# Performance work log

Hardware: AMD Instinct MI355X
Metric: run time of the kernel (lower is better)

## Reference

```python
import jax, jax.numpy as jnp
import numpy as np

B, S, H, NH, HD = 1, 2048, 768, 12, 64   # batch, seq, hidden, heads, head_dim
W = 256                                   # one-sided window (attention_window=512)
NC = S // W                               # query chunks of width W
L, FF, V, G = 12, 3072, 50265, 1          # layers, ffn, vocab, num global tokens (CLS)
HID, EMB = 768, 256                       # head dense size, output embedding size
SCALE = 1.0 / np.sqrt(HD).astype(np.float32)
EPS = 1e-5

def _ln(x, s, b):
    mu = x.mean(-1, keepdims=True)
    xm = x - mu
    v = (xm * xm).mean(-1, keepdims=True)
    return xm * jax.lax.rsqrt(v + EPS) * s + b

def _forward(input_ids, attention_mask, global_attention_mask,
             word_emb, pos_emb, emb_ln_s, emb_ln_b,
             Wq, bq, Wk, bk, Wv, bv, Wqg, bqg, Wkg, bkg, Wvg, bvg, Wo, bo,
             ln1_s, ln1_b, Wf1, bf1, Wf2, bf2, ln2_s, ln2_b,
             dense_w, dense_b, out_w, out_b):
    h = word_emb[input_ids] + pos_emb[None]            # [B,S,H]
    h = _ln(h, emb_ln_s, emb_ln_b)

    key_ok = attention_mask.astype(bool)               # [B,S]
    is_glb = global_attention_mask.astype(bool)        # [B,S]

    # chunked sliding-window machinery: queries in NC chunks of W, each sees 3W keys
    j = jnp.arange(3 * W); qi = jnp.arange(W); c = jnp.arange(NC)
    rel = j[None, :] - qi[:, None]
    band_ok = (rel >= 0) & (rel <= 2 * W)              # |key-query| <= W  -> [W,3W]
    kpos = c[:, None, None] * W + j[None, None, :] - W # abs key position [NC,1,3W]
    in_range = (kpos >= 0) & (kpos < S)
    kposc = jnp.clip(kpos, 0, S - 1)
    # HF removes global tokens from the windowed band (they get dedicated columns)
    kmask = key_ok[:, kposc] & ~is_glb[:, kposc]       # [B,NC,1,3W]
    band_mask = band_ok[None, None] & in_range[None] & kmask          # [B,NC,W,3W]
    gcol_mask = jnp.broadcast_to(key_ok[:, None, None, :G], (B, NC, W, G))
    full_mask = jnp.concatenate([gcol_mask, band_mask], -1)[:, None]  # [B,1,NC,W,G+3W]
    kidx = c[:, None] * W + j[None, :]                 # gather into padded keys [NC,3W]

    def step(h, p):
        q = ((h @ p['Wq'] + p['bq']).reshape(B, NC, W, NH, HD)) * SCALE
        k = (h @ p['Wk'] + p['bk']).reshape(B, S, NH, HD)
        v = (h @ p['Wv'] + p['bv']).reshape(B, S, NH, HD)
        k_ch = jnp.pad(k, ((0, 0), (W, W), (0, 0), (0, 0)))[:, kidx]  # [B,NC,3W,NH,HD]
        v_ch = jnp.pad(v, ((0, 0), (W, W), (0, 0), (0, 0)))[:, kidx]
        s_band = jnp.einsum('bcqnd,bcknd->bncqk', q, k_ch)            # [B,NH,NC,W,3W]
        s_glob = jnp.einsum('bcqnd,bgnd->bncqg', q, k[:, :G])         # [B,NH,NC,W,G]
        scores = jnp.concatenate([s_glob, s_band], -1)
        probs = jax.nn.softmax(jnp.where(full_mask, scores, -1e9), -1)
        pg, pb = probs[..., :G], probs[..., G:]
        out = (jnp.einsum('bncqk,bcknd->bcqnd', pb, v_ch)
               + jnp.einsum('bncqg,bgnd->bcqnd', pg, v[:, :G]))
        out = out.reshape(B, S, NH, HD)
        # global tokens: full attention with dedicated global projections (HF semantics)
        hg = h[:, :G]
        qg = ((hg @ p['Wqg'] + p['bqg']).reshape(B, G, NH, HD)) * SCALE
        kg = (h @ p['Wkg'] + p['bkg']).reshape(B, S, NH, HD)
        vg = (h @ p['Wvg'] + p['bvg']).reshape(B, S, NH, HD)
        sg = jnp.einsum('bgnd,bsnd->bngs', qg, kg)
        ag = jax.nn.softmax(jnp.where(key_ok[:, None, None, :], sg, -1e9), -1)
        og = jnp.einsum('bngs,bsnd->bgnd', ag, vg)
        out = out.at[:, :G].set(og)
        attn = out.reshape(B, S, H) @ p['Wo'] + p['bo']
        h2 = _ln(h + attn, p['ln1_s'], p['ln1_b'])
        ff = jax.nn.gelu(h2 @ p['Wf1'] + p['bf1'], approximate=False) @ p['Wf2'] + p['bf2']
        return _ln(h2 + ff, p['ln2_s'], p['ln2_b']), None

    params = dict(Wq=Wq, bq=bq, Wk=Wk, bk=bk, Wv=Wv, bv=bv, Wqg=Wqg, bqg=bqg,
                  Wkg=Wkg, bkg=bkg, Wvg=Wvg, bvg=bvg, Wo=Wo, bo=bo,
                  ln1_s=ln1_s, ln1_b=ln1_b, Wf1=Wf1, bf1=bf1, Wf2=Wf2, bf2=bf2,
                  ln2_s=ln2_s, ln2_b=ln2_b)
    h, _ = jax.lax.scan(step, h, params)
    pooled = h[:, 0]                                   # CLS token
    y = jnp.tanh(pooled @ dense_w + dense_b)           # dropout = identity (eval)
    return y @ out_w + out_b                           # [B,EMB]

def setup_inputs() -> dict:
    key = jax.random.key(0)
    it = iter(jax.random.split(key, 16))
    def nrm(shape, sd=0.02):
        return jax.random.normal(next(it), shape, jnp.float32) * sd
    return dict(
        input_ids=jax.random.randint(next(it), (B, S), 0, V),
        attention_mask=jnp.ones((B, S), jnp.int32),
        global_attention_mask=jnp.zeros((B, S), jnp.int32).at[:, 0].set(1),
        word_emb=nrm((V, H)), pos_emb=nrm((S, H)),
        emb_ln_s=jnp.ones((H,)), emb_ln_b=jnp.zeros((H,)),
        Wq=nrm((L, H, H)), bq=jnp.zeros((L, H)),
        Wk=nrm((L, H, H)), bk=jnp.zeros((L, H)),
        Wv=nrm((L, H, H)), bv=jnp.zeros((L, H)),
        Wqg=nrm((L, H, H)), bqg=jnp.zeros((L, H)),
        Wkg=nrm((L, H, H)), bkg=jnp.zeros((L, H)),
        Wvg=nrm((L, H, H)), bvg=jnp.zeros((L, H)),
        Wo=nrm((L, H, H)), bo=jnp.zeros((L, H)),
        ln1_s=jnp.ones((L, H)), ln1_b=jnp.zeros((L, H)),
        Wf1=nrm((L, H, FF)), bf1=jnp.zeros((L, FF)),
        Wf2=nrm((L, FF, H)), bf2=jnp.zeros((L, H)),
        ln2_s=jnp.ones((L, H)), ln2_b=jnp.zeros((L, H)),
        dense_w=nrm((H, HID)), dense_b=jnp.zeros((HID,)),
        out_w=nrm((HID, EMB)), out_b=jnp.zeros((EMB,)),
    )

def reference(input_ids, attention_mask, global_attention_mask,
              word_emb, pos_emb, emb_ln_s, emb_ln_b,
              Wq, bq, Wk, bk, Wv, bv, Wqg, bqg, Wkg, bkg, Wvg, bvg, Wo, bo,
              ln1_s, ln1_b, Wf1, bf1, Wf2, bf2, ln2_s, ln2_b,
              dense_w, dense_b, out_w, out_b):
    return _forward(input_ids, attention_mask, global_attention_mask,
                    word_emb, pos_emb, emb_ln_s, emb_ln_b,
                    Wq, bq, Wk, bk, Wv, bv, Wqg, bqg, Wkg, bkg, Wvg, bvg, Wo, bo,
                    ln1_s, ln1_b, Wf1, bf1, Wf2, bf2, ln2_s, ln2_b,
                    dense_w, dense_b, out_w, out_b)
```

## Files before the change

### kernel.cpp

```cpp
#include <hip/hip_runtime.h>
#include <hip/hip_bf16.h>

typedef __hip_bfloat16 bf16;
using bf16x8 = __attribute__((ext_vector_type(8))) short;
using f32x4  = __attribute__((ext_vector_type(4))) float;

#define kNEG 1.0e9f

__device__ __forceinline__ float b2f(bf16 x){ return __bfloat162float(x); }
__device__ __forceinline__ bf16  f2b(float x){ return __float2bfloat16(x); }
__device__ __forceinline__ float us2f(unsigned short u){ return __uint_as_float(((unsigned)u)<<16); }

__device__ __forceinline__ float erf_fast(float z){
  float az = fabsf(z);
  float t = __frcp_rn(fmaf(0.3275911f, az, 1.0f));
  float p = t*fmaf(t, fmaf(t, fmaf(t, fmaf(t, 1.061405429f, -1.453152027f),
                                    1.421413741f), -0.284496736f), 0.254829592f);
  float e = 1.0f - p*__expf(-az*az);
  return copysignf(e, z);
}

#define GLDS16(gp, lp) __builtin_amdgcn_global_load_lds( \
    (const __attribute__((address_space(1))) void*)(gp), \
    (__attribute__((address_space(3))) void*)(lp), 16, 0, 0)

__device__ __forceinline__ void unpack8(uint4 u, float* f){
  f[0]=__uint_as_float(u.x<<16); f[1]=__uint_as_float(u.x&0xffff0000u);
  f[2]=__uint_as_float(u.y<<16); f[3]=__uint_as_float(u.y&0xffff0000u);
  f[4]=__uint_as_float(u.z<<16); f[5]=__uint_as_float(u.z&0xffff0000u);
  f[6]=__uint_as_float(u.w<<16); f[7]=__uint_as_float(u.w&0xffff0000u);
}

__global__ __launch_bounds__(192)
void embed_ln(const int* __restrict__ ids, const float* __restrict__ wemb,
              const float* __restrict__ pemb, const float* __restrict__ lns,
              const float* __restrict__ lnb, float* __restrict__ hout,
              bf16* __restrict__ hbout)
{
  const int row = blockIdx.x;
  const int tid = threadIdx.x;
  const int wave = tid >> 6, lane = tid & 63;
  const int id = ids[row];
  const int i0 = tid*4;
  float4 a = *(const float4*)&wemb[(size_t)id*768 + i0];
  float4 b = *(const float4*)&pemb[(size_t)row*768 + i0];
  float4 x = make_float4(a.x+b.x, a.y+b.y, a.z+b.z, a.w+b.w);
  float s1 = x.x+x.y+x.z+x.w;
  float s2 = x.x*x.x+x.y*x.y+x.z*x.z+x.w*x.w;
  #pragma unroll
  for (int m=32;m>=1;m>>=1){ s1 += __shfl_xor(s1,m); s2 += __shfl_xor(s2,m); }
  __shared__ float red[6];
  if (lane==0){ red[wave]=s1; red[3+wave]=s2; }
  __syncthreads();
  s1 = red[0]+red[1]+red[2];
  s2 = red[3]+red[4]+red[5];
  float mu = s1*(1.0f/768.0f);
  float var = s2*(1.0f/768.0f) - mu*mu;
  float rs = rsqrtf(var + 1e-5f);
  float4 sc = *(const float4*)&lns[i0];
  float4 bi = *(const float4*)&lnb[i0];
  float4 y = make_float4((x.x-mu)*rs*sc.x + bi.x, (x.y-mu)*rs*sc.y + bi.y,
                         (x.z-mu)*rs*sc.z + bi.z, (x.w-mu)*rs*sc.w + bi.w);
  *(float4*)&hout[(size_t)row*768 + i0] = y;
  union { ushort4 u; bf16 h[4]; } pk;
  pk.h[0]=f2b(y.x); pk.h[1]=f2b(y.y); pk.h[2]=f2b(y.z); pk.h[3]=f2b(y.w);
  *(ushort4*)&hbout[(size_t)row*768 + i0] = pk.u;
}

template<int NP>
__global__ __launch_bounds__(192)
void add_ln(const float* __restrict__ res, const bf16* __restrict__ pf,
            const float* __restrict__ lns, const float* __restrict__ lnb,
            float* __restrict__ hout, bf16* __restrict__ hbout)
{
  const size_t MN = (size_t)2048*768;
  const int row = blockIdx.x;
  const int tid = threadIdx.x;
  const int wave = tid >> 6, lane = tid & 63;
  const int i0 = tid*4;
  const size_t base = (size_t)row*768 + i0;
  float4 x = *(const float4*)&res[base];
  #pragma unroll
  for (int p=0;p<NP;p++){
    ushort4 u = *(const ushort4*)&pf[p*MN + base];
    x.x += us2f(u.x); x.y += us2f(u.y); x.z += us2f(u.z); x.w += us2f(u.w);
  }
  float s1 = x.x+x.y+x.z+x.w;
  float s2 = x.x*x.x+x.y*x.y+x.z*x.z+x.w*x.w;
  #pragma unroll
  for (int m=32;m>=1;m>>=1){ s1 += __shfl_xor(s1,m); s2 += __shfl_xor(s2,m); }
  __shared__ float red[6];
  if (lane==0){ red[wave]=s1; red[3+wave]=s2; }
  __syncthreads();
  s1 = red[0]+red[1]+red[2];
  s2 = red[3]+red[4]+red[5];
  float mu = s1*(1.0f/768.0f);
  float var = s2*(1.0f/768.0f) - mu*mu;
  float rs = rsqrtf(var + 1e-5f);
  float4 sc = *(const float4*)&lns[i0];
  float4 bi = *(const float4*)&lnb[i0];
  float4 y = make_float4((x.x-mu)*rs*sc.x + bi.x, (x.y-mu)*rs*sc.y + bi.y,
                         (x.z-mu)*rs*sc.z + bi.z, (x.w-mu)*rs*sc.w + bi.w);
  *(float4*)&hout[base] = y;
  union { ushort4 u; bf16 h[4]; } pk;
  pk.h[0]=f2b(y.x); pk.h[1]=f2b(y.y); pk.h[2]=f2b(y.z); pk.h[3]=f2b(y.w);
  *(ushort4*)&hbout[base] = pk.u;
}

__global__ __launch_bounds__(256)
void prep_all(const float* __restrict__ Wq, const float* __restrict__ Wk,
              const float* __restrict__ Wv, const float* __restrict__ Wkg,
              const float* __restrict__ Wvg, const float* __restrict__ Wo,
              const float* __restrict__ Wf1, const float* __restrict__ Wf2,
              const float* __restrict__ bq, const float* __restrict__ bk,
              const float* __restrict__ bv, const float* __restrict__ bkg,
              const float* __restrict__ bvg,
              bf16* __restrict__ WcatT, bf16* __restrict__ WoT,
              bf16* __restrict__ Wf1T, bf16* __restrict__ Wf2T,
              float* __restrict__ bcat)
{
  const int b = blockIdx.x;
  const int l = blockIdx.y;
  const int tid = threadIdx.x;
  const size_t oHH = (size_t)l*768*768;
  const size_t oHF = (size_t)l*768*3072;
  const size_t oH  = (size_t)l*768;
  if (b >= 504) {
    int i = (b-504)*256 + tid;
    int which = i / 768, j = i - which*768;
    float v;
    if      (which==0) v = bq[oH+j] * 0.125f;
    else if (which==1) v = bk[oH+j];
    else if (which==2) v = bv[oH+j];
    else if (which==3) v = bkg[oH+j];
    else               v = bvg[oH+j];
    bcat[(size_t)l*3840 + i] = v;
    return;
  }
  const float* src; bf16* dst; int N, KT64, p0, tk, k0, n0; float scale = 1.0f;
  if (b < 180) {
    int wsel = b/36, tile = b - wsel*36;
    int tkk = tile/3, tn = tile - tkk*3;
    if      (wsel==0){ src=Wq+oHH;  scale=0.125f; }
    else if (wsel==1){ src=Wk+oHH; }
    else if (wsel==2){ src=Wv+oHH; }
    else if (wsel==3){ src=Wkg+oHH; }
    else             { src=Wvg+oHH; }
    dst = WcatT + (size_t)l*5*768*768;
    N=768; KT64=12; k0=tkk*64; n0=tn*256; p0 = wsel*6 + tn*2; tk = tkk;
  } else if (b < 216) {
    int tile = b-180, tkk = tile/3, tn = tile - tkk*3;
    src = Wo+oHH; dst = WoT + (size_t)l*768*768;
    N=768; KT64=12; k0=tkk*64; n0=tn*256; p0 = tn*2; tk = tkk;
  } else if (b < 360) {
    int tile = b-216, tkk = tile/12, tn = tile - tkk*12;
    src = Wf1+oHF; dst = Wf1T + (size_t)l*768*3072;
    N=3072; KT64=12; k0=tkk*64; n0=tn*256; p0 = tn*2; tk = tkk;
  } else {
    int tile = b-360, tkk = tile/3, tn = tile - tkk*3;
    src = Wf2+oHF; dst = Wf2T + (size_t)l*768*3072;
    N=768; KT64=48; k0=tkk*64; n0=tn*256; p0 = tn*2; tk = tkk;
  }

  __shared__ bf16 t[64][264];
  const int wave = tid>>6, lane = tid&63;
  float4 v[16];
  #pragma unroll
  for (int i=0;i<16;i++){
    int r = i*4 + wave;
    v[i] = *(const float4*)&src[(size_t)(k0+r)*N + n0 + lane*4];
  }
  #pragma unroll
  for (int i=0;i<16;i++){
    int r = i*4 + wave;
    union { ushort4 u; bf16 h[4]; } pk;
    pk.h[0]=f2b(v[i].x*scale); pk.h[1]=f2b(v[i].y*scale);
    pk.h[2]=f2b(v[i].z*scale); pk.h[3]=f2b(v[i].w*scale);
    *(ushort4*)&t[r][lane*4] = pk.u;
  }
  __syncthreads();
  const int rr = tid>>1, half = tid&1;
  const int r7 = rr & 7;
  #pragma unroll
  for (int c=0;c<4;c++){
    const int pp = c>>1, tt = c&1;
    union { uint4 u[2]; bf16 h[16]; } pk;
    #pragma unroll
    for (int j=0;j<16;j++)
      pk.h[j] = t[tt*32 + half*16 + j][pp*128 + rr];
    bf16* base = dst + ((size_t)(p0+pp)*KT64 + tk)*8192 + rr*64;
    const int g0 = tt*4 + half*2;
    *(uint4*)(base + (((g0  ) ^ r7)<<3)) = pk.u[0];
    *(uint4*)(base + (((g0+1) ^ r7)<<3)) = pk.u[1];
  }
}

template<int OUTF, int OUTB, int GELU, int KSPLIT, int VT>
__global__ __launch_bounds__(256)
void gemm_bt(const bf16* __restrict__ A, const bf16* __restrict__ Bt,
             const float* __restrict__ bias,
             bf16* __restrict__ pfb, bf16* __restrict__ outb,
             bf16* __restrict__ vt,
             int M, int N, int K)
{
  __shared__ bf16 As[2][128*64];
  __shared__ bf16 Bs[2][128*64];
  const int tid  = threadIdx.x;
  const int lane = tid & 63;
  const int wave = tid >> 6;
  const int wm = wave >> 1, wn = wave & 1;
  const int gx = gridDim.x, nwg = gx*gridDim.y;
  const int w  = blockIdx.y*gx + blockIdx.x;
  const int cpx = nwg >> 3;
  const int sw = (w & 7)*cpx + (w >> 3);
  const int bm = sw % gx, bn = sw / gx;
  const int bz = (KSPLIT>1) ? blockIdx.z : 0;
  const int fr = lane & 15;
  const int fk = lane >> 4;
  const int x7 = fr & 7;
  const int Ks = K / KSPLIT;
  const int nt = Ks >> 6;
  const int kbeg = bz * Ks;
  const int KT64 = K >> 6;

  const bf16* pa[4];
  int ldsA[4];
  #pragma unroll
  for (int i=0;i<4;i++){
    int s = i*256 + tid;
    int row = s >> 3, k8l = s & 7;
    pa[i] = A + (size_t)(bm*128 + row)*K + kbeg + ((k8l ^ (row&7))<<3);
    ldsA[i] = s*8;
  }
  const bf16* pB = Bt + ((size_t)bn*KT64 + (kbeg>>6))*8192;

  f32x4 acc[4][4];
  const f32x4 zero = {0.f,0.f,0.f,0.f};
  #pragma unroll
  for (int i=0;i<4;i++)
    #pragma unroll
    for (int j=0;j<4;j++) acc[i][j] = zero;

  #pragma unroll
  for (int i=0;i<4;i++) GLDS16(pa[i], &As[0][ldsA[i]]);
  #pragma unroll
  for (int i=0;i<4;i++){ int o=(i*256+tid)*8; GLDS16(pB+o, &Bs[0][o]); }
  if (nt > 1) {
    #pragma unroll
    for (int i=0;i<4;i++) GLDS16(pa[i]+64, &As[1][ldsA[i]]);
    #pragma unroll
    for (int i=0;i<4;i++){ int o=(i*256+tid)*8; GLDS16(pB+8192+o, &Bs[1][o]); }
  }

  for (int t = 0; t < nt; ++t) {
    const int cur = t & 1;
    if (t < nt-1) asm volatile("s_waitcnt vmcnt(8)" ::: "memory");
    else          asm volatile("s_waitcnt vmcnt(0)" ::: "memory");
    __builtin_amdgcn_s_barrier();
    __builtin_amdgcn_sched_barrier(0);

    bf16x8 af[2][4], bfr[2][4];
    #pragma unroll
    for (int kk=0;kk<2;kk++){
      #pragma unroll
      for (int m=0;m<4;m++)
        af[kk][m] = *reinterpret_cast<const bf16x8*>(
            &As[cur][(wm*64 + m*16 + fr)*64 + ((((kk<<2)+fk) ^ x7)<<3)]);
      #pragma unroll
      for (int n=0;n<4;n++)
        bfr[kk][n] = *reinterpret_cast<const bf16x8*>(
            &Bs[cur][(wn*64 + n*16 + fr)*64 + ((((kk<<2)+fk) ^ x7)<<3)]);
    }
    __builtin_amdgcn_s_setprio(1);
    #pragma unroll
    for (int kk=0;kk<2;kk++)
      #pragma unroll
      for (int m=0;m<4;m++)
        #pragma unroll
        for (int n=0;n<4;n++)
          acc[m][n] = __builtin_amdgcn_mfma_f32_16x16x32_bf16(af[kk][m], bfr[kk][n], acc[m][n], 0,0,0);
    __builtin_amdgcn_s_setprio(0);

    __builtin_amdgcn_s_barrier();
    __builtin_amdgcn_sched_barrier(0);
    if (t+2 < nt) {
      #pragma unroll
      for (int i=0;i<4;i++) GLDS16(pa[i] + (size_t)(t+2)*64, &As[cur][ldsA[i]]);
      #pragma unroll
      for (int i=0;i<4;i++){ int o=(i*256+tid)*8;
        GLDS16(pB + (size_t)(t+2)*8192 + o, &Bs[cur][o]); }
    }
  }

  const int row0 = bm*128 + wm*64 + (lane>>4)*4;
  const int col0 = bn*128 + wn*64 + fr;
  bf16* pfz = OUTF ? (pfb + (size_t)bz*M*N) : nullptr;
  #pragma unroll
  for (int n=0;n<4;n++){
    const int col = col0 + n*16;
    const float bv = (bz==0) ? bias[col] : 0.f;
    #pragma unroll
    for (int m=0;m<4;m++){
      const int r0 = row0 + m*16;
      union { ushort4 u; bf16 h[4]; } pk;
      #pragma unroll
      for (int r=0;r<4;r++){
        float x = acc[m][n][r] + bv;
        if (GELU) x = 0.5f*x*(1.0f + erf_fast(x*0.70710678118f));
        size_t idx = (size_t)(r0+r)*N + col;
        pk.h[r] = f2b(x);
        if (OUTF) pfz[idx] = pk.h[r];
        if (OUTB) outb[idx] = pk.h[r];
      }
      if (VT) {
        if (col >= 1536 && col < 2304)
          *(ushort4*)&vt[(size_t)(col-1536)*2048 + r0] = pk.u;
      }
    }
  }
}

__global__ __launch_bounds__(256)
void band_attn(const bf16* __restrict__ qkv, const bf16* __restrict__ Vt,
               const float* __restrict__ h0, const float* __restrict__ Wqg,
               const float* __restrict__ bqg,
               const int* __restrict__ amask, const int* __restrict__ gmask,
               bf16* __restrict__ attn)
{
  const int c = blockIdx.x, n = blockIdx.y, rg = blockIdx.z;
  const int tid = threadIdx.x, wave = tid>>6, lane = tid&63;

  if (rg == 4) {
    if (c != 0) return;
    __shared__ float sg[2048];
    __shared__ float qh[64];
    __shared__ float redg[8];
    __shared__ float partg[4][64];
    {
      const int d = tid & 63;
      const int w = tid >> 6;
      const float* wp = Wqg + (size_t)(w*192)*768 + n*64 + d;
      float a = 0.f;
      #pragma unroll 8
      for (int k=0;k<192;k++) a += h0[w*192+k] * wp[(size_t)k*768];
      partg[w][d] = a;
    }
    __syncthreads();
    if (tid < 64)
      qh[tid] = (partg[0][tid]+partg[1][tid]+partg[2][tid]+partg[3][tid] + bqg[n*64+tid]) * 0.125f;
    __syncthreads();

    float smax = -3.0e38f;
    for (int p=0;p<8;p++){
      int s = p*256 + tid;
      const uint4* kr = (const uint4*)(qkv + (size_t)s*3840 + 2304 + n*64);
      float acc = 0.f;
      #pragma unroll
      for (int d8=0; d8<8; d8++){
        float f[8]; unpack8(kr[d8], f);
        #pragma unroll
        for (int e=0;e<8;e++) acc += f[e]*qh[d8*8+e];
      }
      if (amask[s] == 0) acc = -kNEG;
      sg[s] = acc;
      smax = fmaxf(smax, acc);
    }
    #pragma unroll
    for (int mk=32; mk>=1; mk>>=1) smax = fmaxf(smax, __shfl_xor(smax, mk));
    if (lane==0) redg[wave] = smax;
    __syncthreads();
    smax = fmaxf(fmaxf(redg[0],redg[1]),fmaxf(redg[2],redg[3]));
    float ssum = 0.f;
    for (int p=0;p<8;p++){
      int s = p*256 + tid;
      float e = __expf(sg[s]-smax);
      sg[s] = e;
      ssum += e;
    }
    #pragma unroll
    for (int mk=32; mk>=1; mk>>=1) ssum += __shfl_xor(ssum, mk);
    if (lane==0) redg[4+wave] = ssum;
    __syncthreads();
    float total = redg[4]+redg[5]+redg[6]+redg[7];
    __syncthreads();

    float o0=0.f,o1=0.f,o2=0.f,o3=0.f;
    const int base = wave*512;
    for (int s = base; s < base+512; s+=4){
      o0 += sg[s]   * b2f(qkv[(size_t)s*3840     + 3072 + n*64 + lane]);
      o1 += sg[s+1] * b2f(qkv[(size_t)(s+1)*3840 + 3072 + n*64 + lane]);
      o2 += sg[s+2] * b2f(qkv[(size_t)(s+2)*3840 + 3072 + n*64 + lane]);
      o3 += sg[s+3] * b2f(qkv[(size_t)(s+3)*3840 + 3072 + n*64 + lane]);
    }
    partg[wave][lane] = (o0+o1)+(o2+o3);
    __syncthreads();
    if (tid < 64) {
      float oo = (partg[0][tid]+partg[1][tid]+partg[2][tid]+partg[3][tid]) / total;
      attn[n*64+tid] = f2b(oo);
    }
    return;
  }

  const int fr = lane & 15, fk = lane >> 4;
  const int jj = tid >> 2, seg = tid & 3;

  __shared__ __attribute__((aligned(16))) bf16 q_s[64][72];
  __shared__ __attribute__((aligned(16))) bf16 k_s[2][64][72];
  __shared__ __attribute__((aligned(16))) bf16 vt_s[2][64][72];
  __shared__ __attribute__((aligned(16))) bf16 p_s[4][16][72];
  __shared__ int  okk_s[768];
  __shared__ float kv0[2][64];

  {
    const uint4* src = (const uint4*)(qkv + (size_t)(c*256 + rg*64 + jj)*3840 + n*64 + seg*16);
    *(uint4*)&q_s[jj][seg*16]   = src[0];
    *(uint4*)&q_s[jj][seg*16+8] = src[1];
  }
  #pragma unroll
  for (int p=0;p<3;p++){
    int j = tid + p*256;
    int kpos = c*256 + j - 256;
    int ok = 0;
    if (kpos >= 0 && kpos < 2048) ok = (amask[kpos] != 0) && (gmask[kpos] == 0);
    okk_s[j] = ok;
  }
  if (tid < 64)       kv0[0][tid]    = b2f(qkv[768  + n*64 + tid]);
  else if (tid < 128) kv0[1][tid-64] = b2f(qkv[1536 + n*64 + (tid-64)]);

  auto loadK = [&](int kt, uint4& a, uint4& b){
    int kpos = c*256 + kt*64 + jj - 256;
    int kq = kpos < 0 ? 0 : (kpos > 2047 ? 2047 : kpos);
    const uint4* ks = (const uint4*)(qkv + (size_t)kq*3840 + 768 + n*64 + seg*16);
    a = ks[0]; b = ks[1];
  };
  auto loadV = [&](int kt, uint4& a, uint4& b){
    int base = c*256 + kt*64 - 256;
    int sb = (base < 0 || base > 2048-64) ? 0 : base;
    const uint4* vs = (const uint4*)(Vt + (size_t)(n*64 + jj)*2048 + sb + seg*8);
    a = vs[0]; b = vs[4];
  };

  const int kt_lo = (c==0) ? ((rg > 4) ? rg : 4) : rg;
  int kt_hi = rg+8 < 11 ? rg+8 : 11;
  const int clip = (2303 - c*256) >> 6;
  if (kt_hi > clip) kt_hi = clip;

  uint4 ka,kb,va,vb;
  loadK(kt_lo,ka,kb); loadV(kt_lo,va,vb);
  *(uint4*)&k_s[0][jj][seg*16]    = ka;
  *(uint4*)&k_s[0][jj][seg*16+8]  = kb;
  *(uint4*)&vt_s[0][jj][seg*8]    = va;
  *(uint4*)&vt_s[0][jj][seg*8+32] = vb;

  float lsum[4];
  f32x4 out[4];
  const f32x4 zero = {0.f,0.f,0.f,0.f};
  #pragma unroll
  for (int r=0;r<4;r++) lsum[r] = 0.f;
  #pragma unroll
  for (int dt=0;dt<4;dt++) out[dt] = zero;

  int cur = 0;
  for (int kt = kt_lo; kt <= kt_hi; kt++) {
    const bool pf = (kt < kt_hi);
    if (pf){ loadK(kt+1,ka,kb); loadV(kt+1,va,vb); }
    __syncthreads();

    f32x4 s[4];
    #pragma unroll
    for (int ct=0;ct<4;ct++) s[ct] = zero;
    __builtin_amdgcn_s_setprio(1);
    #pragma unroll
    for (int ks=0;ks<2;ks++){
      bf16x8 aq = *reinterpret_cast<const bf16x8*>(&q_s[wave*16 + fr][ks*32 + fk*8]);
      #pragma unroll
      for (int ct=0;ct<4;ct++){
        bf16x8 bk = *reinterpret_cast<const bf16x8*>(&k_s[cur][ct*16 + fr][ks*32 + fk*8]);
        s[ct] = __builtin_amdgcn_mfma_f32_16x16x32_bf16(aq, bk, s[ct], 0,0,0);
      }
    }
    __builtin_amdgcn_s_setprio(0);
    const int qbase = rg*64 + wave*16 + fk*4;
    #pragma unroll
    for (int ct=0;ct<4;ct++){
      int j = kt*64 + ct*16 + fr;
      int okj = okk_s[j];
      #pragma unroll
      for (int r=0;r<4;r++){
        unsigned rel = (unsigned)(j - (qbase + r));
        float sv = (okj && rel <= 512u) ? s[ct][r] : -kNEG;
        float p = __expf(sv);
        lsum[r] += p;
        p_s[wave][fk*4 + r][ct*16 + fr] = f2b(p);
      }
    }
    __builtin_amdgcn_s_setprio(1);
    #pragma unroll
    for (int ks=0;ks<2;ks++){
      bf16x8 ap = *reinterpret_cast<const bf16x8*>(&p_s[wave][fr][ks*32 + fk*8]);
      #pragma unroll
      for (int dt=0;dt<4;dt++){
        bf16x8 bv = *reinterpret_cast<const bf16x8*>(&vt_s[cur][dt*16 + fr][ks*32 + fk*8]);
        out[dt] = __builtin_amdgcn_mfma_f32_16x16x32_bf16(ap, bv, out[dt], 0,0,0);
      }
    }
    __builtin_amdgcn_s_setprio(0);

    if (pf){
      *(uint4*)&k_s[cur^1][jj][seg*16]    = ka;
      *(uint4*)&k_s[cur^1][jj][seg*16+8]  = kb;
      *(uint4*)&vt_s[cur^1][jj][seg*8]    = va;
      *(uint4*)&vt_s[cur^1][jj][seg*8+32] = vb;
      cur ^= 1;
    }
  }

  const bool okg = (amask[0] != 0);
  #pragma unroll
  for (int r=0;r<4;r++){
    const int row16 = fk*4 + r;
    float ts = lsum[r];
    #pragma unroll
    for (int mk=8; mk>=1; mk>>=1) ts += __shfl_xor(ts, mk);
    float sp = 0.f;
    #pragma unroll
    for (int e=0;e<4;e++){
      int d = fr*4 + e;
      sp += b2f(q_s[wave*16 + row16][d]) * kv0[0][d];
    }
    #pragma unroll
    for (int mk=8; mk>=1; mk>>=1) sp += __shfl_xor(sp, mk);
    float pg = okg ? __expf(sp) : 0.f;
    float lf = ts + pg;
    const int srow = c*256 + rg*64 + wave*16 + row16;
    if (srow != 0) {
      #pragma unroll
      for (int dt=0;dt<4;dt++){
        int d = dt*16 + fr;
        float o = (out[dt][r] + pg*kv0[1][d]) / lf;
        attn[(size_t)srow*768 + n*64 + d] = f2b(o);
      }
    }
  }
}

__global__ __launch_bounds__(256)
void head_p1(const float* __restrict__ h0, const float* __restrict__ dw,
             float* __restrict__ pd)
{
  const int col = blockIdx.x*256 + threadIdx.x;
  const int z = blockIdx.y;
  const int k0 = z*96;
  float acc = 0.f;
  #pragma unroll 8
  for (int k=0;k<96;k++) acc += h0[k0+k]*dw[(size_t)(k0+k)*768 + col];
  pd[z*768 + col] = acc;
}

__global__ __launch_bounds__(256)
void head_p2(const float* __restrict__ pd, const float* __restrict__ db,
             const float* __restrict__ ow, float* __restrict__ po)
{
  __shared__ float yl[96];
  const int tid = threadIdx.x;
  const int z = blockIdx.x;
  const int k0 = z*96;
  if (tid < 96) {
    float a = 0.f;
    #pragma unroll
    for (int zz=0;zz<8;zz++) a += pd[zz*768 + k0 + tid];
    yl[tid] = tanhf(a + db[k0 + tid]);
  }
  __syncthreads();
  const int col = tid;
  float acc = 0.f;
  #pragma unroll 8
  for (int k=0;k<96;k++) acc += yl[k]*ow[(size_t)(k0+k)*256 + col];
  po[z*256 + col] = acc;
}

__global__ __launch_bounds__(256)
void head_fin(const float* __restrict__ po, const float* __restrict__ ob,
              float* __restrict__ out)
{
  const int col = threadIdx.x;
  float a = 0.f;
  #pragma unroll
  for (int z=0;z<8;z++) a += po[z*256 + col];
  out[col] = a + ob[col];
}

extern "C" void kernel_launch(void* const* d_in, const int* in_sizes, int n_in,
                              void* d_out, int out_size, void* d_ws, size_t ws_size,
                              hipStream_t stream)
{
  const int*   ids   = (const int*)d_in[0];
  const int*   amask = (const int*)d_in[1];
  const int*   gmask = (const int*)d_in[2];
  const float* wemb  = (const float*)d_in[3];
  const float* pemb  = (const float*)d_in[4];
  const float* elns  = (const float*)d_in[5];
  const float* elnb  = (const float*)d_in[6];
  const float* Wq    = (const float*)d_in[7];
  const float* bq    = (const float*)d_in[8];
  const float* Wk    = (const float*)d_in[9];
  const float* bk    = (const float*)d_in[10];
  const float* Wv    = (const float*)d_in[11];
  const float* bv    = (const float*)d_in[12];
  const float* Wqg   = (const float*)d_in[13];
  const float* bqg   = (const float*)d_in[14];
  const float* Wkg   = (const float*)d_in[15];
  const float* bkg   = (const float*)d_in[16];
  const float* Wvg   = (const float*)d_in[17];
  const float* bvg   = (const float*)d_in[18];
  const float* Wo    = (const float*)d_in[19];
  const float* bo    = (const float*)d_in[20];
  const float* ln1s  = (const float*)d_in[21];
  const float* ln1b  = (const float*)d_in[22];
  const float* Wf1   = (const float*)d_in[23];
  const float* bf1   = (const float*)d_in[24];
  const float* Wf2   = (const float*)d_in[25];
  const float* bf2   = (const float*)d_in[26];
  const float* ln2s  = (const float*)d_in[27];
  const float* ln2b  = (const float*)d_in[28];
  const float* dw    = (const float*)d_in[29];
  const float* db    = (const float*)d_in[30];
  const float* ow    = (const float*)d_in[31];
  const float* ob    = (const float*)d_in[32];

  char* ws = (char*)d_ws;
  size_t off = 0;
  auto alloc = [&](size_t bytes)->char*{
    char* p = ws + off; off += (bytes + 255) & ~(size_t)255; return p;
  };
  float* h     = (float*)alloc((size_t)2048*768*4);
  bf16*  hb    = (bf16*) alloc((size_t)2048*768*2);
  float* h2    = (float*)alloc((size_t)2048*768*4);
  bf16*  h2b   = (bf16*) alloc((size_t)2048*768*2);
  bf16*  qkv   = (bf16*) alloc((size_t)2048*3840*2);
  bf16*  att   = (bf16*) alloc((size_t)2048*768*2);
  bf16*  f1    = (bf16*) alloc((size_t)2048*3072*2);
  bf16*  Vtb   = (bf16*) alloc((size_t)768*2048*2);
  bf16*  pfb   = (bf16*) alloc((size_t)4*2048*768*2);
  bf16*  WcatT = (bf16*) alloc((size_t)12*5*768*768*2);
  bf16*  WoT   = (bf16*) alloc((size_t)12*768*768*2);
  bf16*  Wf1T  = (bf16*) alloc((size_t)12*768*3072*2);
  bf16*  Wf2T  = (bf16*) alloc((size_t)12*768*3072*2);
  float* bcat  = (float*)alloc((size_t)12*3840*4);
  float* pd    = (float*)alloc((size_t)8*768*4);
  float* po    = (float*)alloc((size_t)8*256*4);

  prep_all<<<dim3(519,12),256,0,stream>>>(Wq, Wk, Wv, Wkg, Wvg, Wo, Wf1, Wf2,
                                          bq, bk, bv, bkg, bvg,
                                          WcatT, WoT, Wf1T, Wf2T, bcat);
  embed_ln<<<2048,192,0,stream>>>(ids, wemb, pemb, elns, elnb, h, hb);

  for (int l=0; l<12; l++) {
    const size_t oHH = (size_t)l*768*768;
    const size_t oH  = (size_t)l*768;
    const size_t oF  = (size_t)l*3072;
    const bf16* WcatT_l = WcatT + (size_t)l*5*768*768;
    const bf16* WoT_l   = WoT   + (size_t)l*768*768;
    const bf16* Wf1T_l  = Wf1T  + (size_t)l*768*3072;
    const bf16* Wf2T_l  = Wf2T  + (size_t)l*768*3072;
    const float* bcat_l = bcat  + (size_t)l*3840;

    gemm_bt<0,1,0,1,1><<<dim3(16,30),256,0,stream>>>(hb, WcatT_l, bcat_l, nullptr, qkv,
                                                     Vtb, 2048, 3840, 768);
    band_attn<<<dim3(8,12,5),256,0,stream>>>(qkv, Vtb, h, Wqg+oHH, bqg+oH,
                                             amask, gmask, att);
    gemm_bt<1,0,0,3,0><<<dim3(16,6,3),256,0,stream>>>(att, WoT_l, bo+oH, pfb, nullptr,
                                                      nullptr, 2048, 768, 768);
    add_ln<3><<<2048,192,0,stream>>>(h, pfb, ln1s+oH, ln1b+oH, h2, h2b);
    gemm_bt<0,1,1,1,0><<<dim3(16,24),256,0,stream>>>(h2b, Wf1T_l, bf1+oF, nullptr, f1,
                                                     nullptr, 2048, 3072, 768);
    gemm_bt<1,0,0,3,0><<<dim3(16,6,3),256,0,stream>>>(f1, Wf2T_l, bf2+oH, pfb, nullptr,
                                                      nullptr, 2048, 768, 3072);
    add_ln<3><<<2048,192,0,stream>>>(h2, pfb, ln2s+oH, ln2b+oH, h, hb);
  }

  head_p1<<<dim3(3,8),256,0,stream>>>(h, dw, pd);
  head_p2<<<8,256,0,stream>>>(pd, db, ow, po);
  head_fin<<<1,256,0,stream>>>(po, ob, (float*)d_out);
}
```

Baseline: 2.114 ms.

## Fold global K/V projections into the CLS global-attention path

Drops the global key and value projections from the fused QKV GEMM, shrinking it from 3840 to 2304 output columns. The single global query row now gets its scores as h·(Wkg·q) plus a bias constant, and its output as Wvg applied to the softmax-weighted sum of h, all computed inside band_attn. This removes a large share of the per-layer projection GEMM and the matching weight preparation. In exchange, 12 single blocks (one per head) must each stream the full fp32 hidden state twice, which may lengthen band_attn's tail. Accumulation order and precision for the global row also change.

```diff
diff --git a/kernel.cpp b/kernel.cpp
--- a/kernel.cpp
+++ b/kernel.cpp
@@ -23,13 +23,6 @@
 #define GLDS16(gp, lp) __builtin_amdgcn_global_load_lds( \
     (const __attribute__((address_space(1))) void*)(gp), \
     (__attribute__((address_space(3))) void*)(lp), 16, 0, 0)
-
-__device__ __forceinline__ void unpack8(uint4 u, float* f){
-  f[0]=__uint_as_float(u.x<<16); f[1]=__uint_as_float(u.x&0xffff0000u);
-  f[2]=__uint_as_float(u.y<<16); f[3]=__uint_as_float(u.y&0xffff0000u);
-  f[4]=__uint_as_float(u.z<<16); f[5]=__uint_as_float(u.z&0xffff0000u);
-  f[6]=__uint_as_float(u.w<<16); f[7]=__uint_as_float(u.w&0xffff0000u);
-}
 
 __global__ __launch_bounds__(192)
 void embed_ln(const int* __restrict__ ids, const float* __restrict__ wemb,
@@ -109,12 +102,10 @@
 
 __global__ __launch_bounds__(256)
 void prep_all(const float* __restrict__ Wq, const float* __restrict__ Wk,
-              const float* __restrict__ Wv, const float* __restrict__ Wkg,
-              const float* __restrict__ Wvg, const float* __restrict__ Wo,
+              const float* __restrict__ Wv, const float* __restrict__ Wo,
               const float* __restrict__ Wf1, const float* __restrict__ Wf2,
               const float* __restrict__ bq, const float* __restrict__ bk,
-              const float* __restrict__ bv, const float* __restrict__ bkg,
-              const float* __restrict__ bvg,
+              const float* __restrict__ bv,
               bf16* __restrict__ WcatT, bf16* __restrict__ WoT,
               bf16* __restrict__ Wf1T, bf16* __restrict__ Wf2T,
               float* __restrict__ bcat)
@@ -125,39 +116,35 @@
   const size_t oHH = (size_t)l*768*768;
   const size_t oHF = (size_t)l*768*3072;
   const size_t oH  = (size_t)l*768;
-  if (b >= 504) {
-    int i = (b-504)*256 + tid;
+  if (b >= 432) {
+    int i = (b-432)*256 + tid;
     int which = i / 768, j = i - which*768;
     float v;
     if      (which==0) v = bq[oH+j] * 0.125f;
     else if (which==1) v = bk[oH+j];
-    else if (which==2) v = bv[oH+j];
-    else if (which==3) v = bkg[oH+j];
-    else               v = bvg[oH+j];
-    bcat[(size_t)l*3840 + i] = v;
+    else               v = bv[oH+j];
+    bcat[(size_t)l*2304 + i] = v;
     return;
   }
   const float* src; bf16* dst; int N, KT64, p0, tk, k0, n0; float scale = 1.0f;
-  if (b < 180) {
+  if (b < 108) {
     int wsel = b/36, tile = b - wsel*36;
     int tkk = tile/3, tn = tile - tkk*3;
     if      (wsel==0){ src=Wq+oHH;  scale=0.125f; }
     else if (wsel==1){ src=Wk+oHH; }
-    else if (wsel==2){ src=Wv+oHH; }
-    else if (wsel==3){ src=Wkg+oHH; }
-    else             { src=Wvg+oHH; }
-    dst = WcatT + (size_t)l*5*768*768;
+    else             { src=Wv+oHH; }
+    dst = WcatT + (size_t)l*3*768*768;
     N=768; KT64=12; k0=tkk*64; n0=tn*256; p0 = wsel*6 + tn*2; tk = tkk;
-  } else if (b < 216) {
-    int tile = b-180, tkk = tile/3, tn = tile - tkk*3;
+  } else if (b < 144) {
+    int tile = b-108, tkk = tile/3, tn = tile - tkk*3;
     src = Wo+oHH; dst = WoT + (size_t)l*768*768;
     N=768; KT64=12; k0=tkk*64; n0=tn*256; p0 = tn*2; tk = tkk;
-  } else if (b < 360) {
-    int tile = b-216, tkk = tile/12, tn = tile - tkk*12;
+  } else if (b < 288) {
+    int tile = b-144, tkk = tile/12, tn = tile - tkk*12;
     src = Wf1+oHF; dst = Wf1T + (size_t)l*768*3072;
     N=3072; KT64=12; k0=tkk*64; n0=tn*256; p0 = tn*2; tk = tkk;
   } else {
-    int tile = b-360, tkk = tile/3, tn = tile - tkk*3;
+    int tile = b-288, tkk = tile/3, tn = tile - tkk*3;
     src = Wf2+oHF; dst = Wf2T + (size_t)l*768*3072;
     N=768; KT64=48; k0=tkk*64; n0=tn*256; p0 = tn*2; tk = tkk;
   }
@@ -322,8 +309,10 @@
 
 __global__ __launch_bounds__(256)
 void band_attn(const bf16* __restrict__ qkv, const bf16* __restrict__ Vt,
-               const float* __restrict__ h0, const float* __restrict__ Wqg,
-               const float* __restrict__ bqg,
+               const float* __restrict__ h0,
+               const float* __restrict__ Wqg, const float* __restrict__ bqg,
+               const float* __restrict__ Wkg, const float* __restrict__ bkg,
+               const float* __restrict__ Wvg, const float* __restrict__ bvg,
                const int* __restrict__ amask, const int* __restrict__ gmask,
                bf16* __restrict__ attn)
 {
@@ -334,6 +323,7 @@
     if (c != 0) return;
     __shared__ float sg[2048];
     __shared__ float qh[64];
+    __shared__ float wz[768];
     __shared__ float redg[8];
     __shared__ float partg[4][64];
     {
@@ -349,17 +339,29 @@
     if (tid < 64)
       qh[tid] = (partg[0][tid]+partg[1][tid]+partg[2][tid]+partg[3][tid] + bqg[n*64+tid]) * 0.125f;
     __syncthreads();
-
+    for (int k = tid; k < 768; k += 256) {
+      const float4* wr = (const float4*)&Wkg[(size_t)k*768 + n*64];
+      float a = 0.f;
+      #pragma unroll
+      for (int d4=0; d4<16; d4++){
+        float4 w4 = wr[d4];
+        a += w4.x*qh[d4*4+0] + w4.y*qh[d4*4+1] + w4.z*qh[d4*4+2] + w4.w*qh[d4*4+3];
+      }
+      wz[k] = a;
+    }
+    float cst = 0.f;
+    #pragma unroll 8
+    for (int d=0; d<64; d++) cst += bkg[n*64+d]*qh[d];
+    __syncthreads();
     float smax = -3.0e38f;
     for (int p=0;p<8;p++){
       int s = p*256 + tid;
-      const uint4* kr = (const uint4*)(qkv + (size_t)s*3840 + 2304 + n*64);
-      float acc = 0.f;
-      #pragma unroll
-      for (int d8=0; d8<8; d8++){
-        float f[8]; unpack8(kr[d8], f);
-        #pragma unroll
-        for (int e=0;e<8;e++) acc += f[e]*qh[d8*8+e];
+      const float4* hr = (const float4*)&h0[(size_t)s*768];
+      float acc = cst;
+      #pragma unroll 4
+      for (int k4=0;k4<192;k4++){
+        float4 h4 = hr[k4];
+        acc += h4.x*wz[k4*4+0] + h4.y*wz[k4*4+1] + h4.z*wz[k4*4+2] + h4.w*wz[k4*4+3];
       }
       if (amask[s] == 0) acc = -kNEG;
       sg[s] = acc;
@@ -383,19 +385,30 @@
     __syncthreads();
     float total = redg[4]+redg[5]+redg[6]+redg[7];
     __syncthreads();
-
-    float o0=0.f,o1=0.f,o2=0.f,o3=0.f;
-    const int base = wave*512;
-    for (int s = base; s < base+512; s+=4){
-      o0 += sg[s]   * b2f(qkv[(size_t)s*3840     + 3072 + n*64 + lane]);
-      o1 += sg[s+1] * b2f(qkv[(size_t)(s+1)*3840 + 3072 + n*64 + lane]);
-      o2 += sg[s+2] * b2f(qkv[(size_t)(s+2)*3840 + 3072 + n*64 + lane]);
-      o3 += sg[s+3] * b2f(qkv[(size_t)(s+3)*3840 + 3072 + n*64 + lane]);
-    }
-    partg[wave][lane] = (o0+o1)+(o2+o3);
+    float z0=0.f,z1=0.f,z2=0.f,y0=0.f,y1=0.f,y2=0.f;
+    const int kk0 = tid*3;
+    for (int s=0;s<2048;s+=2){
+      float a0 = sg[s], a1 = sg[s+1];
+      const float* r0 = &h0[(size_t)s*768 + kk0];
+      const float* r1 = r0 + 768;
+      z0 = fmaf(a0, r0[0], z0); z1 = fmaf(a0, r0[1], z1); z2 = fmaf(a0, r0[2], z2);
+      y0 = fmaf(a1, r1[0], y0); y1 = fmaf(a1, r1[1], y1); y2 = fmaf(a1, r1[2], y2);
+    }
+    wz[kk0+0] = z0+y0; wz[kk0+1] = z1+y1; wz[kk0+2] = z2+y2;
+    __syncthreads();
+    {
+      const int d = tid & 63;
+      const int w = tid >> 6;
+      const float* wv = Wvg + (size_t)(w*192)*768 + n*64 + d;
+      float a = 0.f;
+      #pragma unroll 8
+      for (int k=0;k<192;k++) a = fmaf(wz[w*192+k], wv[(size_t)k*768], a);
+      partg[w][d] = a;
+    }
     __syncthreads();
     if (tid < 64) {
-      float oo = (partg[0][tid]+partg[1][tid]+partg[2][tid]+partg[3][tid]) / total;
+      float oo = (partg[0][tid]+partg[1][tid]+partg[2][tid]+partg[3][tid]) / total
+               + bvg[n*64+tid];
       attn[n*64+tid] = f2b(oo);
     }
     return;
@@ -412,7 +425,7 @@
   __shared__ float kv0[2][64];
 
   {
-    const uint4* src = (const uint4*)(qkv + (size_t)(c*256 + rg*64 + jj)*3840 + n*64 + seg*16);
+    const uint4* src = (const uint4*)(qkv + (size_t)(c*256 + rg*64 + jj)*2304 + n*64 + seg*16);
     *(uint4*)&q_s[jj][seg*16]   = src[0];
     *(uint4*)&q_s[jj][seg*16+8] = src[1];
   }
@@ -430,7 +443,7 @@
   auto loadK = [&](int kt, uint4& a, uint4& b){
     int kpos = c*256 + kt*64 + jj - 256;
     int kq = kpos < 0 ? 0 : (kpos > 2047 ? 2047 : kpos);
-    const uint4* ks = (const uint4*)(qkv + (size_t)kq*3840 + 768 + n*64 + seg*16);
+    const uint4* ks = (const uint4*)(qkv + (size_t)kq*2304 + 768 + n*64 + seg*16);
     a = ks[0]; b = ks[1];
   };
   auto loadV = [&](int kt, uint4& a, uint4& b){
@@ -637,21 +650,21 @@
   bf16*  hb    = (bf16*) alloc((size_t)2048*768*2);
   float* h2    = (float*)alloc((size_t)2048*768*4);
   bf16*  h2b   = (bf16*) alloc((size_t)2048*768*2);
-  bf16*  qkv   = (bf16*) alloc((size_t)2048*3840*2);
+  bf16*  qkv   = (bf16*) alloc((size_t)2048*2304*2);
   bf16*  att   = (bf16*) alloc((size_t)2048*768*2);
   bf16*  f1    = (bf16*) alloc((size_t)2048*3072*2);
   bf16*  Vtb   = (bf16*) alloc((size_t)768*2048*2);
   bf16*  pfb   = (bf16*) alloc((size_t)4*2048*768*2);
-  bf16*  WcatT = (bf16*) alloc((size_t)12*5*768*768*2);
+  bf16*  WcatT = (bf16*) alloc((size_t)12*3*768*768*2);
   bf16*  WoT   = (bf16*) alloc((size_t)12*768*768*2);
   bf16*  Wf1T  = (bf16*) alloc((size_t)12*768*3072*2);
   bf16*  Wf2T  = (bf16*) alloc((size_t)12*768*3072*2);
-  float* bcat  = (float*)alloc((size_t)12*3840*4);
+  float* bcat  = (float*)alloc((size_t)12*2304*4);
   float* pd    = (float*)alloc((size_t)8*768*4);
   float* po    = (float*)alloc((size_t)8*256*4);
 
-  prep_all<<<dim3(519,12),256,0,stream>>>(Wq, Wk, Wv, Wkg, Wvg, Wo, Wf1, Wf2,
-                                          bq, bk, bv, bkg, bvg,
+  prep_all<<<dim3(441,12),256,0,stream>>>(Wq, Wk, Wv, Wo, Wf1, Wf2,
+                                          bq, bk, bv,
                                           WcatT, WoT, Wf1T, Wf2T, bcat);
   embed_ln<<<2048,192,0,stream>>>(ids, wemb, pemb, elns, elnb, h, hb);
 
@@ -659,15 +672,17 @@
     const size_t oHH = (size_t)l*768*768;
     const size_t oH  = (size_t)l*768;
     const size_t oF  = (size_t)l*3072;
-    const bf16* WcatT_l = WcatT + (size_t)l*5*768*768;
+    const bf16* WcatT_l = WcatT + (size_t)l*3*768*768;
     const bf16* WoT_l   = WoT   + (size_t)l*768*768;
     const bf16* Wf1T_l  = Wf1T  + (size_t)l*768*3072;
     const bf16* Wf2T_l  = Wf2T  + (size_t)l*768*3072;
-    const float* bcat_l = bcat  + (size_t)l*3840;
-
-    gemm_bt<0,1,0,1,1><<<dim3(16,30),256,0,stream>>>(hb, WcatT_l, bcat_l, nullptr, qkv,
-                                                     Vtb, 2048, 3840, 768);
-    band_attn<<<dim3(8,12,5),256,0,stream>>>(qkv, Vtb, h, Wqg+oHH, bqg+oH,
+    const float* bcat_l = bcat  + (size_t)l*2304;
+
+    gemm_bt<0,1,0,1,1><<<dim3(16,18),256,0,stream>>>(hb, WcatT_l, bcat_l, nullptr, qkv,
+                                                     Vtb, 2048, 2304, 768);
+    band_attn<<<dim3(8,12,5),256,0,stream>>>(qkv, Vtb, h,
+                                             Wqg+oHH, bqg+oH, Wkg+oHH, bkg+oH,
+                                             Wvg+oHH, bvg+oH,
                                              amask, gmask, att);
     gemm_bt<1,0,0,3,0><<<dim3(16,6,3),256,0,stream>>>(att, WoT_l, bo+oH, pfb, nullptr,
                                                       nullptr, 2048, 768, 768);
```

Result: slower. 4.933 ms (+133.3%).
